# Performance work log

Hardware: AMD Instinct MI355X
Metric: run time of the kernel (lower is better)

The kernel has to match this reference:

```python
import jax, jax.numpy as jnp
import numpy as np

BN_EPS = 1e-5
NORM_EPS = 1e-12  # F.normalize eps


def setup_inputs() -> dict:
    key = jax.random.key(0)
    ks = jax.random.split(key, 4)
    B, C1, H, W = 32, 2048, 32, 32
    D1, D2, NC = 1024, 256, 1000
    x = jax.random.normal(ks[0], (B, C1, H, W), dtype=jnp.float32)
    w1 = jax.random.normal(ks[1], (D1, C1), dtype=jnp.float32) * 0.01  # init_weights normal 0.01
    gamma = jnp.ones((D1,), dtype=jnp.float32)
    beta = jnp.zeros((D1,), dtype=jnp.float32)
    w2 = jax.random.normal(ks[2], (D2, D1), dtype=jnp.float32) * 0.01
    prototypes = jax.random.normal(ks[3], (NC, D2), dtype=jnp.float32)
    return {"x": x, "w1": w1, "gamma": gamma, "beta": beta, "w2": w2, "prototypes": prototypes}


def _l2_normalize(v, axis):
    n = jnp.sqrt(jnp.sum(v * v, axis=axis, keepdims=True))
    return v / jnp.maximum(n, NORM_EPS)


def reference(x, w1, gamma, beta, w2, prototypes):
    # 1x1 conv (no bias) == channel matmul
    h = jnp.einsum('bchw,dc->bdhw', x, w1)  # [B,D1,H,W]
    # BatchNorm2d (training-mode batch stats, affine)
    mean = jnp.mean(h, axis=(0, 2, 3), keepdims=True)
    var = jnp.var(h, axis=(0, 2, 3), keepdims=True)
    h = (h - mean) * jax.lax.rsqrt(var + BN_EPS)
    h = h * gamma[None, :, None, None] + beta[None, :, None, None]
    h = jax.nn.relu(h)
    # final 1x1 conv
    f = jnp.einsum('bchw,dc->bdhw', h, w2)  # [B,D2,H,W]
    B, D, H, W = f.shape
    f = f.reshape(B, D, H * W)  # flatten(2)
    # L2-normalize over channel dim per spatial position, and prototypes per row
    f_norm = _l2_normalize(f, axis=1)           # [B,D,HW]
    p_norm = _l2_normalize(prototypes, axis=1)  # [N,D]
    # einsum('bdc,nd->bnc').sum(-1) == contract d then sum c in one fused einsum
    sim = jnp.einsum('bdc,nd->bn', f_norm, p_norm)  # [B,N]
    return sim
```

## Files before the change

### kernel.cpp

```cpp
#include <hip/hip_runtime.h>

typedef __bf16 bf16;
typedef __bf16 bf16x4 __attribute__((ext_vector_type(4)));
typedef __bf16 bf16x8 __attribute__((ext_vector_type(8)));
typedef float  f32x4  __attribute__((ext_vector_type(4)));

__device__ inline void async_copy16(void* lds, const void* g) {
  __builtin_amdgcn_global_load_lds((const __attribute__((address_space(1))) void*)g,
                                   (__attribute__((address_space(3))) void*)lds,
                                   16, 0, 0);
}

__global__ __launch_bounds__(256)
void f2bf_kernel(const float* __restrict__ in, bf16* __restrict__ out, int n4) {
  int i = blockIdx.x * 256 + threadIdx.x;
  if (i < n4) {
    float4 v = ((const float4*)in)[i];
    bf16x4 o;
    o[0] = (bf16)v.x; o[1] = (bf16)v.y; o[2] = (bf16)v.z; o[3] = (bf16)v.w;
    ((bf16x4*)out)[i] = o;
  }
}

__global__ __launch_bounds__(256)
void transpose_convert(const float* __restrict__ x, bf16* __restrict__ xb) {
  __shared__ float tile[64][65];
  const int tx = threadIdx.x & 15;
  const int ty = threadIdx.x >> 4;
  const int b   = blockIdx.z;
  const int c0  = blockIdx.y * 64;
  const int hw0 = blockIdx.x * 64;
  const float* xp = x + ((size_t)b * 2048 + c0) * 1024 + hw0;
#pragma unroll
  for (int i = 0; i < 4; ++i) {
    const int c = i * 16 + ty;
    const float4 v = *(const float4*)(xp + (size_t)c * 1024 + tx * 4);
    tile[c][tx * 4 + 0] = v.x; tile[c][tx * 4 + 1] = v.y;
    tile[c][tx * 4 + 2] = v.z; tile[c][tx * 4 + 3] = v.w;
  }
  __syncthreads();
  bf16* op = xb + ((size_t)b * 1024 + hw0) * 2048 + c0;
#pragma unroll
  for (int i = 0; i < 4; ++i) {
    const int hw = i * 16 + ty;
    bf16x4 o;
    o[0] = (bf16)tile[tx * 4 + 0][hw];
    o[1] = (bf16)tile[tx * 4 + 1][hw];
    o[2] = (bf16)tile[tx * 4 + 2][hw];
    o[3] = (bf16)tile[tx * 4 + 3][hw];
    *(bf16x4*)(op + (size_t)hw * 2048 + tx * 4) = o;
  }
}

__global__ __launch_bounds__(256, 4)
void gemm1(const bf16* __restrict__ A, const bf16* __restrict__ Bt,
           bf16* __restrict__ Cb, float* __restrict__ S1, float* __restrict__ S2) {
  __shared__ __align__(16) bf16 As[128 * 64];
  __shared__ __align__(16) bf16 Bs[128 * 64];
  const int K = 2048, N = 1024;
  const int tid  = threadIdx.x;
  const int wave = tid >> 6;
  const int lane = tid & 63;
  const int id = blockIdx.x;
  const int bm = (id & 7) * 32 + ((id >> 3) >> 3);
  const int bn = (id >> 3) & 7;
  const int wr = wave >> 1, wc = wave & 1;
  const int srow = lane >> 3;
  const int scol = (lane & 7) ^ srow;

  f32x4 acc[4][4];
#pragma unroll
  for (int r = 0; r < 4; ++r)
#pragma unroll
    for (int c = 0; c < 4; ++c) acc[r][c] = (f32x4){0.f, 0.f, 0.f, 0.f};

  const bf16* Ag = A + (size_t)(bm * 128) * K;
  const bf16* Bg = Bt + (size_t)(bn * 128) * K;

  const int mrow = lane & 15;
  const int kq = lane >> 4;
  const int sw = mrow & 7;
  const bf16* Asw = As + (wr * 64) * 64;
  const bf16* Bsw = Bs + (wc * 64) * 64;

  for (int k0 = 0; k0 < K; k0 += 64) {
#pragma unroll
    for (int j = 0; j < 4; ++j) {
      const int row = j * 32 + wave * 8;
      async_copy16((void*)(As + row * 64),
                   (const void*)(Ag + (size_t)(row + srow) * K + k0 + scol * 8));
      async_copy16((void*)(Bs + row * 64),
                   (const void*)(Bg + (size_t)(row + srow) * K + k0 + scol * 8));
    }
    __syncthreads();
#pragma unroll
    for (int kk = 0; kk < 2; ++kk) {
      bf16x8 af[4], bfr[4];
      const int lc = kk * 4 + kq;
#pragma unroll
      for (int r = 0; r < 4; ++r)
        af[r] = *(const bf16x8*)(Asw + (r * 16 + mrow) * 64 + ((lc ^ sw) * 8));
#pragma unroll
      for (int c = 0; c < 4; ++c)
        bfr[c] = *(const bf16x8*)(Bsw + (c * 16 + mrow) * 64 + ((lc ^ sw) * 8));
#pragma unroll
      for (int r = 0; r < 4; ++r)
#pragma unroll
        for (int c = 0; c < 4; ++c)
          acc[r][c] = __builtin_amdgcn_mfma_f32_16x16x32_bf16(af[r], bfr[c], acc[r][c], 0, 0, 0);
    }
    __syncthreads();
  }

  const int crow = (lane >> 4) * 4;
  const int ccol = lane & 15;
#pragma unroll
  for (int r = 0; r < 4; ++r)
#pragma unroll
    for (int c = 0; c < 4; ++c)
#pragma unroll
      for (int i = 0; i < 4; ++i) {
        const int gm = bm * 128 + wr * 64 + r * 16 + crow + i;
        const int gn = bn * 128 + wc * 64 + c * 16 + ccol;
        Cb[(size_t)gm * N + gn] = (bf16)acc[r][c][i];
      }

  float s1[4], s2[4];
#pragma unroll
  for (int c = 0; c < 4; ++c) {
    float a = 0.f, b = 0.f;
#pragma unroll
    for (int r = 0; r < 4; ++r)
#pragma unroll
      for (int i = 0; i < 4; ++i) { const float v = acc[r][c][i]; a += v; b += v * v; }
#pragma unroll
    for (int msk = 16; msk < 64; msk <<= 1) { a += __shfl_xor(a, msk, 64); b += __shfl_xor(b, msk, 64); }
    s1[c] = a; s2[c] = b;
  }
  float* S1s = (float*)As;
  float* S2s = S1s + 256;
  if ((lane & 15) == lane) {
#pragma unroll
    for (int c = 0; c < 4; ++c) {
      S1s[wr * 128 + wc * 64 + c * 16 + lane] = s1[c];
      S2s[wr * 128 + wc * 64 + c * 16 + lane] = s2[c];
    }
  }
  __syncthreads();
  if (tid < 128) {
    atomicAdd(&S1[bn * 128 + tid], S1s[tid] + S1s[128 + tid]);
    atomicAdd(&S2[bn * 128 + tid], S2s[tid] + S2s[128 + tid]);
  }
}

__global__ __launch_bounds__(256)
void bn_finalize(const float* __restrict__ S1, const float* __restrict__ S2,
                 const float* __restrict__ gamma, const float* __restrict__ beta,
                 float* __restrict__ scale, float* __restrict__ shift) {
  const int d = blockIdx.x * 256 + threadIdx.x;
  const float inv_n = 1.0f / 32768.0f;
  const float mean = S1[d] * inv_n;
  const float var  = S2[d] * inv_n - mean * mean;
  const float rstd = rsqrtf(var + 1e-5f);
  const float sc = gamma[d] * rstd;
  scale[d] = sc;
  shift[d] = beta[d] - mean * sc;
}

__global__ __launch_bounds__(512, 2)
void gemm2f(const bf16* __restrict__ A, const bf16* __restrict__ Bt,
            const float* __restrict__ scale, const float* __restrict__ shift,
            float* __restrict__ g) {
  __shared__ __align__(16) bf16 As[128 * 64];
  __shared__ __align__(16) bf16 Bs[256 * 64];
  const int K = 1024;
  const int tid  = threadIdx.x;
  const int wave = tid >> 6;
  const int lane = tid & 63;
  const int bm = blockIdx.x;
  const int wr = wave >> 2, wc = wave & 3;
  const int srow = lane >> 3;
  const int scol = (lane & 7) ^ srow;

  f32x4 acc[4][4];
#pragma unroll
  for (int r = 0; r < 4; ++r)
#pragma unroll
    for (int c = 0; c < 4; ++c) acc[r][c] = (f32x4){0.f, 0.f, 0.f, 0.f};

  const bf16* Ag = A + (size_t)(bm * 128) * K;

  const int mrow = lane & 15;
  const int kq = lane >> 4;
  const int sw = mrow & 7;
  const bf16* Asw = As + (wr * 64) * 64;
  const bf16* Bsw = Bs + (wc * 64) * 64;

  for (int k0 = 0; k0 < K; k0 += 64) {
#pragma unroll
    for (int j = 0; j < 2; ++j) {
      const int row = wave * 16 + j * 8;
      async_copy16((void*)(As + row * 64),
                   (const void*)(Ag + (size_t)(row + srow) * K + k0 + scol * 8));
    }
#pragma unroll
    for (int j = 0; j < 4; ++j) {
      const int row = wave * 32 + j * 8;
      async_copy16((void*)(Bs + row * 64),
                   (const void*)(Bt + (size_t)(row + srow) * K + k0 + scol * 8));
    }
    __syncthreads();
#pragma unroll
    for (int kk = 0; kk < 2; ++kk) {
      const int lc = kk * 4 + kq;
      const int kbase = k0 + lc * 8;
      const float4 sc0 = *(const float4*)(scale + kbase);
      const float4 sc1 = *(const float4*)(scale + kbase + 4);
      const float4 sh0 = *(const float4*)(shift + kbase);
      const float4 sh1 = *(const float4*)(shift + kbase + 4);
      const float scv[8] = {sc0.x, sc0.y, sc0.z, sc0.w, sc1.x, sc1.y, sc1.z, sc1.w};
      const float shv[8] = {sh0.x, sh0.y, sh0.z, sh0.w, sh1.x, sh1.y, sh1.z, sh1.w};
      bf16x8 af[4], bfr[4];
#pragma unroll
      for (int r = 0; r < 4; ++r) {
        bf16x8 a = *(const bf16x8*)(Asw + (r * 16 + mrow) * 64 + ((lc ^ sw) * 8));
#pragma unroll
        for (int j = 0; j < 8; ++j)
          a[j] = (bf16)fmaxf(0.f, fmaf((float)a[j], scv[j], shv[j]));
        af[r] = a;
      }
#pragma unroll
      for (int c = 0; c < 4; ++c)
        bfr[c] = *(const bf16x8*)(Bsw + (c * 16 + mrow) * 64 + ((lc ^ sw) * 8));
#pragma unroll
      for (int r = 0; r < 4; ++r)
#pragma unroll
        for (int c = 0; c < 4; ++c)
          acc[r][c] = __builtin_amdgcn_mfma_f32_16x16x32_bf16(af[r], bfr[c], acc[r][c], 0, 0, 0);
    }
    __syncthreads();
  }

  float* ss4   = (float*)As;
  float* inv_s = ss4 + 512;
  const int q = lane >> 4;
#pragma unroll
  for (int r = 0; r < 4; ++r) {
    float ssv[4];
#pragma unroll
    for (int i = 0; i < 4; ++i) {
      float s = 0.f;
#pragma unroll
      for (int c = 0; c < 4; ++c) { const float v = acc[r][c][i]; s += v * v; }
#pragma unroll
      for (int msk = 1; msk < 16; msk <<= 1) s += __shfl_xor(s, msk, 64);
      ssv[i] = s;
    }
    if ((lane & 15) == 0)
#pragma unroll
      for (int i = 0; i < 4; ++i)
        ss4[wc * 128 + wr * 64 + r * 16 + q * 4 + i] = ssv[i];
  }
  __syncthreads();
  if (tid < 128) {
    const float rs = ss4[tid] + ss4[128 + tid] + ss4[256 + tid] + ss4[384 + tid];
    inv_s[tid] = 1.0f / fmaxf(sqrtf(rs), 1e-12f);
  }
  __syncthreads();
  const int b = bm >> 3;
  const int ccol = lane & 15;
#pragma unroll
  for (int c = 0; c < 4; ++c) {
    float gl = 0.f;
#pragma unroll
    for (int r = 0; r < 4; ++r)
#pragma unroll
      for (int i = 0; i < 4; ++i)
        gl += acc[r][c][i] * inv_s[wr * 64 + r * 16 + q * 4 + i];
#pragma unroll
    for (int msk = 16; msk < 64; msk <<= 1) gl += __shfl_xor(gl, msk, 64);
    if ((lane & 48) == 0)
      atomicAdd(&g[b * 256 + wc * 64 + c * 16 + ccol], gl);
  }
}

__global__ __launch_bounds__(256)
void sim_kernel(const float* __restrict__ g, const float* __restrict__ protos,
                float* __restrict__ out) {
  const int wave = threadIdx.x >> 6, lane = threadIdx.x & 63;
  const int n = blockIdx.x * 4 + wave;
  const float4 p = *(const float4*)(protos + (size_t)n * 256 + lane * 4);
  float ss = p.x * p.x + p.y * p.y + p.z * p.z + p.w * p.w;
#pragma unroll
  for (int msk = 1; msk < 64; msk <<= 1) ss += __shfl_xor(ss, msk, 64);
  const float inv = 1.0f / fmaxf(sqrtf(ss), 1e-12f);
  const float px = p.x * inv, py = p.y * inv, pz = p.z * inv, pw = p.w * inv;
  for (int b = 0; b < 32; ++b) {
    const float4 gv = *(const float4*)(g + b * 256 + lane * 4);
    float d = px * gv.x + py * gv.y + pz * gv.z + pw * gv.w;
#pragma unroll
    for (int msk = 1; msk < 64; msk <<= 1) d += __shfl_xor(d, msk, 64);
    if (lane == 0) out[b * 1000 + n] = d;
  }
}

extern "C" void kernel_launch(void* const* d_in, const int* in_sizes, int n_in,
                              void* d_out, int out_size, void* d_ws, size_t ws_size,
                              hipStream_t stream) {
  const float* x      = (const float*)d_in[0];
  const float* w1     = (const float*)d_in[1];
  const float* gamma  = (const float*)d_in[2];
  const float* beta   = (const float*)d_in[3];
  const float* w2     = (const float*)d_in[4];
  const float* protos = (const float*)d_in[5];
  float* out = (float*)d_out;

  char* ws = (char*)d_ws;
  bf16*  xb    = (bf16*)(ws);
  bf16*  hb    = (bf16*)(ws + (size_t)134217728);
  bf16*  w1b   = (bf16*)(ws + (size_t)201326592);
  bf16*  w2b   = (bf16*)(ws + (size_t)205520896);
  float* S1    = (float*)(ws + (size_t)206045184);
  float* S2    = (float*)(ws + (size_t)206049280);
  float* g     = (float*)(ws + (size_t)206053376);
  float* scale = (float*)(ws + (size_t)206086144);
  float* shift = (float*)(ws + (size_t)206090240);

  hipMemsetAsync(S1, 0, 40960, stream);

  f2bf_kernel<<<2048, 256, 0, stream>>>(w1, w1b, 524288);
  f2bf_kernel<<<256, 256, 0, stream>>>(w2, w2b, 65536);
  transpose_convert<<<dim3(16, 32, 32), 256, 0, stream>>>(x, xb);
  gemm1<<<2048, 256, 0, stream>>>(xb, w1b, hb, S1, S2);
  bn_finalize<<<4, 256, 0, stream>>>(S1, S2, gamma, beta, scale, shift);
  gemm2f<<<256, 512, 0, stream>>>(hb, w2b, scale, shift, g);
  sim_kernel<<<250, 256, 0, stream>>>(g, protos, out);
}
```

Before: 609.7 us.

## Fuse BN finalize into gemm2f and retile to 64-row blocks

Removes the separate bn_finalize launch. Each gemm2f block now computes BN scale and shift from S1/S2/gamma/beta into shared memory and reads them from LDS instead of global memory. The gemm2f tile shrinks from 128 to 64 rows with 256 threads, doubling the grid to 512 blocks, and the normalization reduction is simplified accordingly. This saves a kernel launch and the global scale/shift round trip. The costs are redundant finalize work in every block, more LDS per block, and re-loading the full B tile for twice as many blocks.

Result: no change. 598.4 us (-1.9%).

```diff
diff --git a/kernel.cpp b/kernel.cpp
--- a/kernel.cpp
+++ b/kernel.cpp
@@ -153,59 +153,63 @@
   }
 }
 
-__global__ __launch_bounds__(256)
-void bn_finalize(const float* __restrict__ S1, const float* __restrict__ S2,
-                 const float* __restrict__ gamma, const float* __restrict__ beta,
-                 float* __restrict__ scale, float* __restrict__ shift) {
-  const int d = blockIdx.x * 256 + threadIdx.x;
-  const float inv_n = 1.0f / 32768.0f;
-  const float mean = S1[d] * inv_n;
-  const float var  = S2[d] * inv_n - mean * mean;
-  const float rstd = rsqrtf(var + 1e-5f);
-  const float sc = gamma[d] * rstd;
-  scale[d] = sc;
-  shift[d] = beta[d] - mean * sc;
-}
-
-__global__ __launch_bounds__(512, 2)
+__global__ __launch_bounds__(256, 2)
 void gemm2f(const bf16* __restrict__ A, const bf16* __restrict__ Bt,
-            const float* __restrict__ scale, const float* __restrict__ shift,
+            const float* __restrict__ S1, const float* __restrict__ S2,
+            const float* __restrict__ gamma, const float* __restrict__ beta,
             float* __restrict__ g) {
-  __shared__ __align__(16) bf16 As[128 * 64];
+  __shared__ __align__(16) bf16 As[64 * 64];
   __shared__ __align__(16) bf16 Bs[256 * 64];
+  __shared__ __align__(16) float scale_s[1024];
+  __shared__ __align__(16) float shift_s[1024];
   const int K = 1024;
   const int tid  = threadIdx.x;
   const int wave = tid >> 6;
   const int lane = tid & 63;
   const int bm = blockIdx.x;
-  const int wr = wave >> 2, wc = wave & 3;
+  const int wc = wave;
   const int srow = lane >> 3;
   const int scol = (lane & 7) ^ srow;
 
+  {
+    const float inv_n = 1.0f / 32768.0f;
+    const float4 s1 = ((const float4*)S1)[tid];
+    const float4 s2 = ((const float4*)S2)[tid];
+    const float4 ga = ((const float4*)gamma)[tid];
+    const float4 be = ((const float4*)beta)[tid];
+    float4 sc, sh;
+    float m, v, rs;
+    m = s1.x * inv_n; v = s2.x * inv_n - m * m; rs = rsqrtf(v + 1e-5f); sc.x = ga.x * rs; sh.x = be.x - m * sc.x;
+    m = s1.y * inv_n; v = s2.y * inv_n - m * m; rs = rsqrtf(v + 1e-5f); sc.y = ga.y * rs; sh.y = be.y - m * sc.y;
+    m = s1.z * inv_n; v = s2.z * inv_n - m * m; rs = rsqrtf(v + 1e-5f); sc.z = ga.z * rs; sh.z = be.z - m * sc.z;
+    m = s1.w * inv_n; v = s2.w * inv_n - m * m; rs = rsqrtf(v + 1e-5f); sc.w = ga.w * rs; sh.w = be.w - m * sc.w;
+    ((float4*)scale_s)[tid] = sc;
+    ((float4*)shift_s)[tid] = sh;
+  }
+
   f32x4 acc[4][4];
 #pragma unroll
   for (int r = 0; r < 4; ++r)
 #pragma unroll
     for (int c = 0; c < 4; ++c) acc[r][c] = (f32x4){0.f, 0.f, 0.f, 0.f};
 
-  const bf16* Ag = A + (size_t)(bm * 128) * K;
+  const bf16* Ag = A + (size_t)(bm * 64) * K;
 
   const int mrow = lane & 15;
   const int kq = lane >> 4;
   const int sw = mrow & 7;
-  const bf16* Asw = As + (wr * 64) * 64;
   const bf16* Bsw = Bs + (wc * 64) * 64;
 
   for (int k0 = 0; k0 < K; k0 += 64) {
 #pragma unroll
     for (int j = 0; j < 2; ++j) {
-      const int row = wave * 16 + j * 8;
+      const int row = j * 32 + wave * 8;
       async_copy16((void*)(As + row * 64),
                    (const void*)(Ag + (size_t)(row + srow) * K + k0 + scol * 8));
     }
 #pragma unroll
-    for (int j = 0; j < 4; ++j) {
-      const int row = wave * 32 + j * 8;
+    for (int j = 0; j < 8; ++j) {
+      const int row = j * 32 + wave * 8;
       async_copy16((void*)(Bs + row * 64),
                    (const void*)(Bt + (size_t)(row + srow) * K + k0 + scol * 8));
     }
@@ -214,16 +218,16 @@
     for (int kk = 0; kk < 2; ++kk) {
       const int lc = kk * 4 + kq;
       const int kbase = k0 + lc * 8;
-      const float4 sc0 = *(const float4*)(scale + kbase);
-      const float4 sc1 = *(const float4*)(scale + kbase + 4);
-      const float4 sh0 = *(const float4*)(shift + kbase);
-      const float4 sh1 = *(const float4*)(shift + kbase + 4);
+      const float4 sc0 = *(const float4*)(scale_s + kbase);
+      const float4 sc1 = *(const float4*)(scale_s + kbase + 4);
+      const float4 sh0 = *(const float4*)(shift_s + kbase);
+      const float4 sh1 = *(const float4*)(shift_s + kbase + 4);
       const float scv[8] = {sc0.x, sc0.y, sc0.z, sc0.w, sc1.x, sc1.y, sc1.z, sc1.w};
       const float shv[8] = {sh0.x, sh0.y, sh0.z, sh0.w, sh1.x, sh1.y, sh1.z, sh1.w};
       bf16x8 af[4], bfr[4];
 #pragma unroll
       for (int r = 0; r < 4; ++r) {
-        bf16x8 a = *(const bf16x8*)(Asw + (r * 16 + mrow) * 64 + ((lc ^ sw) * 8));
+        bf16x8 a = *(const bf16x8*)(As + (r * 16 + mrow) * 64 + ((lc ^ sw) * 8));
 #pragma unroll
         for (int j = 0; j < 8; ++j)
           a[j] = (bf16)fmaxf(0.f, fmaf((float)a[j], scv[j], shv[j]));
@@ -242,7 +246,7 @@
   }
 
   float* ss4   = (float*)As;
-  float* inv_s = ss4 + 512;
+  float* inv_s = ss4 + 256;
   const int q = lane >> 4;
 #pragma unroll
   for (int r = 0; r < 4; ++r) {
@@ -259,15 +263,15 @@
     if ((lane & 15) == 0)
 #pragma unroll
       for (int i = 0; i < 4; ++i)
-        ss4[wc * 128 + wr * 64 + r * 16 + q * 4 + i] = ssv[i];
+        ss4[wc * 64 + r * 16 + q * 4 + i] = ssv[i];
   }
   __syncthreads();
-  if (tid < 128) {
-    const float rs = ss4[tid] + ss4[128 + tid] + ss4[256 + tid] + ss4[384 + tid];
+  if (tid < 64) {
+    const float rs = ss4[tid] + ss4[64 + tid] + ss4[128 + tid] + ss4[192 + tid];
     inv_s[tid] = 1.0f / fmaxf(sqrtf(rs), 1e-12f);
   }
   __syncthreads();
-  const int b = bm >> 3;
+  const int b = bm >> 4;
   const int ccol = lane & 15;
 #pragma unroll
   for (int c = 0; c < 4; ++c) {
@@ -276,7 +280,7 @@
     for (int r = 0; r < 4; ++r)
 #pragma unroll
       for (int i = 0; i < 4; ++i)
-        gl += acc[r][c][i] * inv_s[wr * 64 + r * 16 + q * 4 + i];
+        gl += acc[r][c][i] * inv_s[r * 16 + q * 4 + i];
 #pragma unroll
     for (int msk = 16; msk < 64; msk <<= 1) gl += __shfl_xor(gl, msk, 64);
     if ((lane & 48) == 0)
@@ -323,8 +327,6 @@
   float* S1    = (float*)(ws + (size_t)206045184);
   float* S2    = (float*)(ws + (size_t)206049280);
   float* g     = (float*)(ws + (size_t)206053376);
-  float* scale = (float*)(ws + (size_t)206086144);
-  float* shift = (float*)(ws + (size_t)206090240);
 
   hipMemsetAsync(S1, 0, 40960, stream);
 
@@ -332,7 +334,6 @@
   f2bf_kernel<<<256, 256, 0, stream>>>(w2, w2b, 65536);
   transpose_convert<<<dim3(16, 32, 32), 256, 0, stream>>>(x, xb);
   gemm1<<<2048, 256, 0, stream>>>(xb, w1b, hb, S1, S2);
-  bn_finalize<<<4, 256, 0, stream>>>(S1, S2, gamma, beta, scale, shift);
-  gemm2f<<<256, 512, 0, stream>>>(hb, w2b, scale, shift, g);
+  gemm2f<<<512, 256, 0, stream>>>(hb, w2b, S1, S2, gamma, beta, g);
   sim_kernel<<<250, 256, 0, stream>>>(g, protos, out);
 }
```
